# Performance work log

Measured on AMD Instinct MI355X. Metric: run time of the kernel, lower is better.

## Reference

```python
import jax, jax.numpy as jnp
import numpy as np
from jax.scipy.special import gammaln, logsumexp

D = 64
K = 32
ALPHA0 = 1000.0
N = 50000
LOG2PI = float(np.log(2.0 * np.pi))


def setup_inputs() -> dict:
    key = jax.random.key(0)
    k1, k2, k3, k4 = jax.random.split(key, 4)
    x = jax.random.normal(k1, (N, D), dtype=jnp.float32)
    # theta = [p (simplex), mu, sigma (>0)] matching theta_from_zeta's output constraints
    p = jax.nn.softmax(jax.random.normal(k2, (K,), dtype=jnp.float32))
    mu = jax.random.normal(k3, (K * D,), dtype=jnp.float32)
    sigma = jnp.exp(0.3 * jax.random.normal(k4, (K * D,), dtype=jnp.float32))
    theta = jnp.concatenate([p, mu, sigma])
    return {"x": x, "theta": theta, "full_data_size": 500000}


def reference(x, theta, full_data_size):
    # Unpack theta exactly as GMM.log_prob does
    p = theta[:K]                                  # [K]
    mu = theta[K:K + K * D].reshape(K, D)          # [K, D]
    sigma = theta[K + K * D:K + 2 * K * D].reshape(K, D)  # [K, D]

    # Per-sample, per-component Gaussian log-prob, fused via matmuls:
    # sum_d (x_id - mu_kd)^2 / sigma_kd^2
    inv_var = 1.0 / (sigma * sigma)                # [K, D]
    quad = ((x * x) @ inv_var.T
            - 2.0 * (x @ (mu * inv_var).T)
            + jnp.sum(mu * mu * inv_var, axis=1))  # [N, K]
    log_norm = -jnp.sum(jnp.log(sigma), axis=1) - 0.5 * D * LOG2PI  # [K]
    comp = jnp.log(p) + log_norm - 0.5 * quad      # [N, K]

    ll = jnp.sum(logsumexp(comp, axis=1)) * (full_data_size / x.shape[0])

    # Priors (same as torch.distributions Normal/Dirichlet/LogNormal log_prob)
    prior_mu = jnp.sum(-0.5 * mu * mu - 0.5 * LOG2PI)
    a = ALPHA0
    prior_p = jnp.sum((a - 1.0) * jnp.log(p)) + gammaln(K * a) - K * gammaln(a)
    log_sig = jnp.log(sigma)
    prior_sigma = jnp.sum(-log_sig - 0.5 * LOG2PI - 0.5 * log_sig * log_sig)

    return ll + prior_mu + prior_p + prior_sigma
```

## Files before the change

### kernel.cpp

```cpp
#include <hip/hip_runtime.h>
#include <hip/hip_bf16.h>
#include <math.h>

namespace {
constexpr int GD = 64;
constexpr int GK = 32;
constexpr float LOG2PI_F = 1.8378770664093454f;

typedef __attribute__((ext_vector_type(8))) short bf16x8;
typedef __attribute__((ext_vector_type(4))) float f32x4;

__device__ __forceinline__ short f2bf(float f) {
  __hip_bfloat16 h = __float2bfloat16(f);
  return __builtin_bit_cast(short, h);
}

__device__ __forceinline__ float4 sq4(const float4 a) {
  return make_float4(a.x * a.x, a.y * a.y, a.z * a.z, a.w * a.w);
}

__device__ __forceinline__ bf16x8 pack8(const float4 a, const float4 b) {
  bf16x8 r;
  r[0] = f2bf(a.x); r[1] = f2bf(a.y); r[2] = f2bf(a.z); r[3] = f2bf(a.w);
  r[4] = f2bf(b.x); r[5] = f2bf(b.y); r[6] = f2bf(b.z); r[7] = f2bf(b.w);
  return r;
}

__global__ __launch_bounds__(256) void gmm_main(
    const float* __restrict__ x, const float* __restrict__ theta,
    float* __restrict__ ws, int n) {
  __shared__ bf16x8 frag[4][4][32];
  __shared__ float pls[8][32];
  __shared__ float pmm[8][32];
  __shared__ float Asm[GK];
  __shared__ float bred[4];

  const int t = threadIdx.x;
  const int lane = t & 63;
  const int wave = t >> 6;
  const int c1 = lane & 15;
  const int g = lane >> 4;
  const int dlo = g * 8;
  const int dhi = 32 + g * 8;

  const int base = blockIdx.x * 256 + wave * 64;
  float4 xv[4][4];
#pragma unroll
  for (int tt = 0; tt < 4; ++tt) {
    const int r = base + tt * 16 + c1;
    const size_t o = (size_t)(r < n ? r : n - 1) * GD;
    xv[tt][0] = *(const float4*)(x + o + dlo);
    xv[tt][1] = *(const float4*)(x + o + dlo + 4);
    xv[tt][2] = *(const float4*)(x + o + dhi);
    xv[tt][3] = *(const float4*)(x + o + dhi + 4);
  }

  {
    const int c = t & 31;
    const int gh = t >> 5;
    const int gg = gh & 3;
    const int hf = gh >> 2;
    const int d0 = hf * 32 + gg * 8;
    const float* __restrict__ mu = theta + GK + c * GD + d0;
    const float* __restrict__ sg = theta + GK + GK * GD + c * GD + d0;
    const float4 m0 = *(const float4*)(mu);
    const float4 m1 = *(const float4*)(mu + 4);
    const float4 s0 = *(const float4*)(sg);
    const float4 s1 = *(const float4*)(sg + 4);
    const float mv[8] = {m0.x, m0.y, m0.z, m0.w, m1.x, m1.y, m1.z, m1.w};
    const float sv[8] = {s0.x, s0.y, s0.z, s0.w, s1.x, s1.y, s1.z, s1.w};
    bf16x8 f1, f2;
    float ls = 0.f, mm = 0.f;
#pragma unroll
    for (int j = 0; j < 8; ++j) {
      const float iv = __builtin_amdgcn_rcpf(sv[j] * sv[j]);
      const float l = __logf(sv[j]);
      ls += l;
      mm = fmaf(mv[j] * mv[j], iv, mm);
      f1[j] = f2bf(mv[j] * iv);
      f2[j] = f2bf(-0.5f * iv);
    }
    frag[hf][gg][c] = f1;
    frag[hf + 2][gg][c] = f2;
    pls[gh][c] = ls;
    pmm[gh][c] = mm;
  }
  __syncthreads();
  if (t < GK) {
    float ls = 0.f, mm = 0.f;
#pragma unroll
    for (int i = 0; i < 8; ++i) { ls += pls[i][t]; mm += pmm[i][t]; }
    Asm[t] = __logf(theta[t]) - ls - 0.5f * GD * LOG2PI_F - 0.5f * mm;
  }
  __syncthreads();

  const bf16x8 W0l = frag[0][g][c1], W0h = frag[0][g][c1 + 16];
  const bf16x8 W1l = frag[1][g][c1], W1h = frag[1][g][c1 + 16];
  const bf16x8 W2l = frag[2][g][c1], W2h = frag[2][g][c1 + 16];
  const bf16x8 W3l = frag[3][g][c1], W3h = frag[3][g][c1 + 16];
  float asl[4], ash[4];
#pragma unroll
  for (int j = 0; j < 4; ++j) {
    asl[j] = Asm[g * 4 + j];
    ash[j] = Asm[16 + g * 4 + j];
  }

  float rowacc = 0.f;
#pragma unroll
  for (int tt = 0; tt < 4; ++tt) {
    const bf16x8 b0 = pack8(xv[tt][0], xv[tt][1]);
    const bf16x8 b1 = pack8(xv[tt][2], xv[tt][3]);
    const bf16x8 b2 = pack8(sq4(xv[tt][0]), sq4(xv[tt][1]));
    const bf16x8 b3 = pack8(sq4(xv[tt][2]), sq4(xv[tt][3]));
    f32x4 D0 = {0.f, 0.f, 0.f, 0.f};
    f32x4 D1 = {0.f, 0.f, 0.f, 0.f};
    D0 = __builtin_amdgcn_mfma_f32_16x16x32_bf16(W0l, b0, D0, 0, 0, 0);
    D1 = __builtin_amdgcn_mfma_f32_16x16x32_bf16(W0h, b0, D1, 0, 0, 0);
    D0 = __builtin_amdgcn_mfma_f32_16x16x32_bf16(W1l, b1, D0, 0, 0, 0);
    D1 = __builtin_amdgcn_mfma_f32_16x16x32_bf16(W1h, b1, D1, 0, 0, 0);
    D0 = __builtin_amdgcn_mfma_f32_16x16x32_bf16(W2l, b2, D0, 0, 0, 0);
    D1 = __builtin_amdgcn_mfma_f32_16x16x32_bf16(W2h, b2, D1, 0, 0, 0);
    D0 = __builtin_amdgcn_mfma_f32_16x16x32_bf16(W3l, b3, D0, 0, 0, 0);
    D1 = __builtin_amdgcn_mfma_f32_16x16x32_bf16(W3h, b3, D1, 0, 0, 0);

    const float e0 = D0[0] + asl[0], e1 = D0[1] + asl[1];
    const float e2 = D0[2] + asl[2], e3 = D0[3] + asl[3];
    const float e4 = D1[0] + ash[0], e5 = D1[1] + ash[1];
    const float e6 = D1[2] + ash[2], e7 = D1[3] + ash[3];
    float m = fmaxf(fmaxf(fmaxf(e0, e1), fmaxf(e2, e3)),
                    fmaxf(fmaxf(e4, e5), fmaxf(e6, e7)));
    m = fmaxf(m, __shfl_xor(m, 16));
    m = fmaxf(m, __shfl_xor(m, 32));
    float e = (__expf(e0 - m) + __expf(e1 - m)) + (__expf(e2 - m) + __expf(e3 - m)) +
              (__expf(e4 - m) + __expf(e5 - m)) + (__expf(e6 - m) + __expf(e7 - m));
    e += __shfl_xor(e, 16);
    e += __shfl_xor(e, 32);
    const int r = base + tt * 16 + c1;
    rowacc += (r < n) ? (m + __logf(e)) : 0.f;
  }

  float v = (g == 0) ? rowacc : 0.f;
  v += __shfl_xor(v, 1);
  v += __shfl_xor(v, 2);
  v += __shfl_xor(v, 4);
  v += __shfl_xor(v, 8);
  if (lane == 0) bred[wave] = v;
  __syncthreads();
  if (t == 0) ws[blockIdx.x] = (bred[0] + bred[1]) + (bred[2] + bred[3]);
}

__global__ __launch_bounds__(256) void gmm_tail(const float* __restrict__ theta,
                                                const int* __restrict__ fds,
                                                const float* __restrict__ ws,
                                                float* __restrict__ out,
                                                float gterm, int n, int nblk) {
  const int t = threadIdx.x;
  float acc = 0.f;
  for (int i = t; i < nblk; i += 256) acc += ws[i];
  acc *= (float)fds[0] / (float)n;
  const int k = t >> 3, jj = t & 7;
  float pr = 0.f;
#pragma unroll
  for (int i = 0; i < 8; ++i) {
    const int idx = k * GD + jj * 8 + i;
    const float mu = theta[GK + idx];
    const float sgv = theta[GK + GK * GD + idx];
    const float ls = __logf(sgv);
    pr += -0.5f * mu * mu - ls - 0.5f * ls * ls - LOG2PI_F;
  }
  if (jj == 0) pr += 999.0f * __logf(theta[k]);
  acc += pr;
  __shared__ float red[256];
  red[t] = acc;
  __syncthreads();
  for (int off = 128; off > 0; off >>= 1) {
    if (t < off) red[t] += red[t + off];
    __syncthreads();
  }
  if (t == 0) out[0] = red[0] + gterm;
}
}

extern "C" void kernel_launch(void* const* d_in, const int* in_sizes, int n_in,
                              void* d_out, int out_size, void* d_ws, size_t ws_size,
                              hipStream_t stream) {
  const float* x = (const float*)d_in[0];
  const float* theta = (const float*)d_in[1];
  const int* fds = (const int*)d_in[2];
  float* out = (float*)d_out;
  float* ws = (float*)d_ws;
  const int n = in_sizes[0] / GD;
  const int nblk = (n + 255) / 256;
  const float gterm = (float)(lgamma(32.0 * 1000.0) - 32.0 * lgamma(1000.0));

  gmm_main<<<nblk, 256, 0, stream>>>(x, theta, ws, n);
  gmm_tail<<<1, 256, 0, stream>>>(theta, fds, ws, out, gterm, n, nblk);
}
```

Before: 12.73 us.

## Use 1024-thread blocks with one row tile per wave and fold priors into main

The main kernel now launches 1024 threads per block, with each wave processing one 16-row tile instead of four, which spreads the per-row work across more waves to expose parallelism and memory-level concurrency. Block 0 computes the prior terms during its theta folding pass and writes them to the workspace, so the tail kernel only sums block partials with shuffles. In exchange, each block repeats the theta folding done by its first 256 threads while the other waves wait at barriers. The tail now assumes nblk is at most 256.

```diff
diff --git a/kernel.cpp b/kernel.cpp
--- a/kernel.cpp
+++ b/kernel.cpp
@@ -26,14 +26,15 @@
   return r;
 }
 
-__global__ __launch_bounds__(256) void gmm_main(
+__global__ __launch_bounds__(1024) void gmm_main(
     const float* __restrict__ x, const float* __restrict__ theta,
-    float* __restrict__ ws, int n) {
+    float* __restrict__ ws, int n, int nblk) {
   __shared__ bf16x8 frag[4][4][32];
   __shared__ float pls[8][32];
   __shared__ float pmm[8][32];
   __shared__ float Asm[GK];
-  __shared__ float bred[4];
+  __shared__ float bred[16];
+  __shared__ float pprior[5];
 
   const int t = threadIdx.x;
   const int lane = t & 63;
@@ -42,35 +43,35 @@
   const int g = lane >> 4;
   const int dlo = g * 8;
   const int dhi = 32 + g * 8;
-
-  const int base = blockIdx.x * 256 + wave * 64;
-  float4 xv[4][4];
-#pragma unroll
-  for (int tt = 0; tt < 4; ++tt) {
-    const int r = base + tt * 16 + c1;
-    const size_t o = (size_t)(r < n ? r : n - 1) * GD;
-    xv[tt][0] = *(const float4*)(x + o + dlo);
-    xv[tt][1] = *(const float4*)(x + o + dlo + 4);
-    xv[tt][2] = *(const float4*)(x + o + dhi);
-    xv[tt][3] = *(const float4*)(x + o + dhi + 4);
-  }
-
-  {
-    const int c = t & 31;
-    const int gh = t >> 5;
-    const int gg = gh & 3;
-    const int hf = gh >> 2;
-    const int d0 = hf * 32 + gg * 8;
+  const bool folder = (t < 256);
+
+  float4 m0, m1, s0, s1;
+  int c = 0, gh = 0;
+  if (folder) {
+    c = t & 31;
+    gh = t >> 5;
+    const int d0 = (gh >> 2) * 32 + (gh & 3) * 8;
     const float* __restrict__ mu = theta + GK + c * GD + d0;
     const float* __restrict__ sg = theta + GK + GK * GD + c * GD + d0;
-    const float4 m0 = *(const float4*)(mu);
-    const float4 m1 = *(const float4*)(mu + 4);
-    const float4 s0 = *(const float4*)(sg);
-    const float4 s1 = *(const float4*)(sg + 4);
+    m0 = *(const float4*)(mu);
+    m1 = *(const float4*)(mu + 4);
+    s0 = *(const float4*)(sg);
+    s1 = *(const float4*)(sg + 4);
+  }
+
+  const int base = blockIdx.x * 256 + wave * 16;
+  const int rA = base + c1;
+  const size_t oA = (size_t)(rA < n ? rA : n - 1) * GD;
+  const float4 xA0 = *(const float4*)(x + oA + dlo);
+  const float4 xA1 = *(const float4*)(x + oA + dlo + 4);
+  const float4 xA2 = *(const float4*)(x + oA + dhi);
+  const float4 xA3 = *(const float4*)(x + oA + dhi + 4);
+
+  if (folder) {
     const float mv[8] = {m0.x, m0.y, m0.z, m0.w, m1.x, m1.y, m1.z, m1.w};
     const float sv[8] = {s0.x, s0.y, s0.z, s0.w, s1.x, s1.y, s1.z, s1.w};
     bf16x8 f1, f2;
-    float ls = 0.f, mm = 0.f;
+    float ls = 0.f, mm = 0.f, pr = 0.f;
 #pragma unroll
     for (int j = 0; j < 8; ++j) {
       const float iv = __builtin_amdgcn_rcpf(sv[j] * sv[j]);
@@ -79,18 +80,33 @@
       mm = fmaf(mv[j] * mv[j], iv, mm);
       f1[j] = f2bf(mv[j] * iv);
       f2[j] = f2bf(-0.5f * iv);
+      pr += -0.5f * mv[j] * mv[j] - l - 0.5f * l * l - LOG2PI_F;
     }
+    const int gg = gh & 3;
+    const int hf = gh >> 2;
     frag[hf][gg][c] = f1;
     frag[hf + 2][gg][c] = f2;
     pls[gh][c] = ls;
     pmm[gh][c] = mm;
+    if (blockIdx.x == 0) {
+#pragma unroll
+      for (int off = 1; off < 64; off <<= 1) pr += __shfl_xor(pr, off);
+      if (lane == 0) pprior[wave] = pr;
+    }
   }
   __syncthreads();
   if (t < GK) {
     float ls = 0.f, mm = 0.f;
 #pragma unroll
     for (int i = 0; i < 8; ++i) { ls += pls[i][t]; mm += pmm[i][t]; }
-    Asm[t] = __logf(theta[t]) - ls - 0.5f * GD * LOG2PI_F - 0.5f * mm;
+    const float lp = __logf(theta[t]);
+    Asm[t] = lp - ls - 0.5f * GD * LOG2PI_F - 0.5f * mm;
+    if (blockIdx.x == 0) {
+      float plp = 999.0f * lp;
+#pragma unroll
+      for (int off = 1; off < 32; off <<= 1) plp += __shfl_xor(plp, off);
+      if (t == 0) pprior[4] = plp;
+    }
   }
   __syncthreads();
 
@@ -105,79 +121,66 @@
     ash[j] = Asm[16 + g * 4 + j];
   }
 
-  float rowacc = 0.f;
-#pragma unroll
-  for (int tt = 0; tt < 4; ++tt) {
-    const bf16x8 b0 = pack8(xv[tt][0], xv[tt][1]);
-    const bf16x8 b1 = pack8(xv[tt][2], xv[tt][3]);
-    const bf16x8 b2 = pack8(sq4(xv[tt][0]), sq4(xv[tt][1]));
-    const bf16x8 b3 = pack8(sq4(xv[tt][2]), sq4(xv[tt][3]));
-    f32x4 D0 = {0.f, 0.f, 0.f, 0.f};
-    f32x4 D1 = {0.f, 0.f, 0.f, 0.f};
-    D0 = __builtin_amdgcn_mfma_f32_16x16x32_bf16(W0l, b0, D0, 0, 0, 0);
-    D1 = __builtin_amdgcn_mfma_f32_16x16x32_bf16(W0h, b0, D1, 0, 0, 0);
-    D0 = __builtin_amdgcn_mfma_f32_16x16x32_bf16(W1l, b1, D0, 0, 0, 0);
-    D1 = __builtin_amdgcn_mfma_f32_16x16x32_bf16(W1h, b1, D1, 0, 0, 0);
-    D0 = __builtin_amdgcn_mfma_f32_16x16x32_bf16(W2l, b2, D0, 0, 0, 0);
-    D1 = __builtin_amdgcn_mfma_f32_16x16x32_bf16(W2h, b2, D1, 0, 0, 0);
-    D0 = __builtin_amdgcn_mfma_f32_16x16x32_bf16(W3l, b3, D0, 0, 0, 0);
-    D1 = __builtin_amdgcn_mfma_f32_16x16x32_bf16(W3h, b3, D1, 0, 0, 0);
-
-    const float e0 = D0[0] + asl[0], e1 = D0[1] + asl[1];
-    const float e2 = D0[2] + asl[2], e3 = D0[3] + asl[3];
-    const float e4 = D1[0] + ash[0], e5 = D1[1] + ash[1];
-    const float e6 = D1[2] + ash[2], e7 = D1[3] + ash[3];
-    float m = fmaxf(fmaxf(fmaxf(e0, e1), fmaxf(e2, e3)),
-                    fmaxf(fmaxf(e4, e5), fmaxf(e6, e7)));
-    m = fmaxf(m, __shfl_xor(m, 16));
-    m = fmaxf(m, __shfl_xor(m, 32));
-    float e = (__expf(e0 - m) + __expf(e1 - m)) + (__expf(e2 - m) + __expf(e3 - m)) +
-              (__expf(e4 - m) + __expf(e5 - m)) + (__expf(e6 - m) + __expf(e7 - m));
-    e += __shfl_xor(e, 16);
-    e += __shfl_xor(e, 32);
-    const int r = base + tt * 16 + c1;
-    rowacc += (r < n) ? (m + __logf(e)) : 0.f;
-  }
-
-  float v = (g == 0) ? rowacc : 0.f;
+  const bf16x8 b0 = pack8(xA0, xA1);
+  const bf16x8 b1 = pack8(xA2, xA3);
+  const bf16x8 b2 = pack8(sq4(xA0), sq4(xA1));
+  const bf16x8 b3 = pack8(sq4(xA2), sq4(xA3));
+  f32x4 D0 = {0.f, 0.f, 0.f, 0.f};
+  f32x4 D1 = {0.f, 0.f, 0.f, 0.f};
+  D0 = __builtin_amdgcn_mfma_f32_16x16x32_bf16(W0l, b0, D0, 0, 0, 0);
+  D1 = __builtin_amdgcn_mfma_f32_16x16x32_bf16(W0h, b0, D1, 0, 0, 0);
+  D0 = __builtin_amdgcn_mfma_f32_16x16x32_bf16(W1l, b1, D0, 0, 0, 0);
+  D1 = __builtin_amdgcn_mfma_f32_16x16x32_bf16(W1h, b1, D1, 0, 0, 0);
+  D0 = __builtin_amdgcn_mfma_f32_16x16x32_bf16(W2l, b2, D0, 0, 0, 0);
+  D1 = __builtin_amdgcn_mfma_f32_16x16x32_bf16(W2h, b2, D1, 0, 0, 0);
+  D0 = __builtin_amdgcn_mfma_f32_16x16x32_bf16(W3l, b3, D0, 0, 0, 0);
+  D1 = __builtin_amdgcn_mfma_f32_16x16x32_bf16(W3h, b3, D1, 0, 0, 0);
+
+  const float e0 = D0[0] + asl[0], e1 = D0[1] + asl[1];
+  const float e2 = D0[2] + asl[2], e3 = D0[3] + asl[3];
+  const float e4 = D1[0] + ash[0], e5 = D1[1] + ash[1];
+  const float e6 = D1[2] + ash[2], e7 = D1[3] + ash[3];
+  float m = fmaxf(fmaxf(fmaxf(e0, e1), fmaxf(e2, e3)),
+                  fmaxf(fmaxf(e4, e5), fmaxf(e6, e7)));
+  m = fmaxf(m, __shfl_xor(m, 16));
+  m = fmaxf(m, __shfl_xor(m, 32));
+  float e = (__expf(e0 - m) + __expf(e1 - m)) + (__expf(e2 - m) + __expf(e3 - m)) +
+            (__expf(e4 - m) + __expf(e5 - m)) + (__expf(e6 - m) + __expf(e7 - m));
+  e += __shfl_xor(e, 16);
+  e += __shfl_xor(e, 32);
+  const float lA = m + __logf(e);
+
+  float v = (g == 0 && rA < n) ? lA : 0.f;
   v += __shfl_xor(v, 1);
   v += __shfl_xor(v, 2);
   v += __shfl_xor(v, 4);
   v += __shfl_xor(v, 8);
   if (lane == 0) bred[wave] = v;
   __syncthreads();
-  if (t == 0) ws[blockIdx.x] = (bred[0] + bred[1]) + (bred[2] + bred[3]);
-}
-
-__global__ __launch_bounds__(256) void gmm_tail(const float* __restrict__ theta,
-                                                const int* __restrict__ fds,
+  if (t == 0) {
+    float s = 0.f;
+#pragma unroll
+    for (int i = 0; i < 16; ++i) s += bred[i];
+    ws[blockIdx.x] = s;
+    if (blockIdx.x == 0)
+      ws[nblk] = (pprior[0] + pprior[1]) + (pprior[2] + pprior[3]) + pprior[4];
+  }
+}
+
+__global__ __launch_bounds__(256) void gmm_tail(const int* __restrict__ fds,
                                                 const float* __restrict__ ws,
                                                 float* __restrict__ out,
                                                 float gterm, int n, int nblk) {
   const int t = threadIdx.x;
-  float acc = 0.f;
-  for (int i = t; i < nblk; i += 256) acc += ws[i];
+  float acc = (t < nblk) ? ws[t] : 0.f;
   acc *= (float)fds[0] / (float)n;
-  const int k = t >> 3, jj = t & 7;
-  float pr = 0.f;
-#pragma unroll
-  for (int i = 0; i < 8; ++i) {
-    const int idx = k * GD + jj * 8 + i;
-    const float mu = theta[GK + idx];
-    const float sgv = theta[GK + GK * GD + idx];
-    const float ls = __logf(sgv);
-    pr += -0.5f * mu * mu - ls - 0.5f * ls * ls - LOG2PI_F;
-  }
-  if (jj == 0) pr += 999.0f * __logf(theta[k]);
-  acc += pr;
-  __shared__ float red[256];
-  red[t] = acc;
-  __syncthreads();
-  for (int off = 128; off > 0; off >>= 1) {
-    if (t < off) red[t] += red[t + off];
-    __syncthreads();
-  }
-  if (t == 0) out[0] = red[0] + gterm;
+  if (t == 0) acc += ws[nblk] + gterm;
+#pragma unroll
+  for (int off = 1; off < 64; off <<= 1) acc += __shfl_xor(acc, off);
+  __shared__ float red[4];
+  if ((t & 63) == 0) red[t >> 6] = acc;
+  __syncthreads();
+  if (t == 0) out[0] = (red[0] + red[1]) + (red[2] + red[3]);
 }
 }
 
@@ -193,6 +196,6 @@
   const int nblk = (n + 255) / 256;
   const float gterm = (float)(lgamma(32.0 * 1000.0) - 32.0 * lgamma(1000.0));
 
-  gmm_main<<<nblk, 256, 0, stream>>>(x, theta, ws, n);
-  gmm_tail<<<1, 256, 0, stream>>>(theta, fds, ws, out, gterm, n, nblk);
-}
+  gmm_main<<<nblk, 1024, 0, stream>>>(x, theta, ws, n, nblk);
+  gmm_tail<<<1, 256, 0, stream>>>(fds, ws, out, gterm, n, nblk);
+}
```

After: 11.33 us. -11.0%, faster.
